# Performance work log

Measured on AMD Instinct MI355X. Metric: run time of the kernel, lower is better.

## Reference

```python
import jax, jax.numpy as jnp
import numpy as np

N = 50000
E = 800000
IN_DIM = 128
HID = 64


def _glorot(key, shape):
    fan_in, fan_out = shape[0], shape[-1]
    lim = jnp.sqrt(6.0 / (fan_in + fan_out))
    return jax.random.uniform(key, shape, jnp.float32, -lim, lim)


def setup_inputs() -> dict:
    key = jax.random.key(0)
    ks = jax.random.split(key, 12)
    x = jax.random.normal(ks[0], (N, IN_DIM), jnp.float32)
    edge_index = jax.random.randint(ks[1], (2, E), 0, N, jnp.int64)
    return {
        "x": x,
        "edge_index": edge_index,
        # GATConv 1: in=128 -> 64 per head, 4 heads (concat -> 256)
        "W1": _glorot(ks[2], (IN_DIM, 4 * HID)),
        "a_src1": _glorot(ks[3], (4, HID)),
        "a_dst1": _glorot(ks[4], (4, HID)),
        "b1": jnp.zeros((4 * HID,), jnp.float32),
        # GATConv 2: in=256 -> 64, 1 head
        "W2": _glorot(ks[5], (4 * HID, HID)),
        "a_src2": _glorot(ks[6], (1, HID)),
        "a_dst2": _glorot(ks[7], (1, HID)),
        "b2": jnp.zeros((HID,), jnp.float32),
        # classifier 64 -> 32 -> 2
        "W3": _glorot(ks[8], (HID, 32)),
        "b3": jnp.zeros((32,), jnp.float32),
        "W4": _glorot(ks[9], (32, 2)),
        "b4": jnp.zeros((2,), jnp.float32),
    }


def _gat_layer(x, edge_index, W, a_src, a_dst, b, heads, out_ch):
    """PyG-style GATConv (add_self_loops=True, negative_slope=0.2, concat)."""
    n = x.shape[0]
    loop = jnp.arange(n, dtype=edge_index.dtype)
    src = jnp.concatenate([edge_index[0], loop])  # [E+N]
    dst = jnp.concatenate([edge_index[1], loop])
    h = (x @ W).reshape(n, heads, out_ch)  # [N,H,C]
    as_ = jnp.sum(h * a_src[None], axis=-1)  # [N,H]
    ad_ = jnp.sum(h * a_dst[None], axis=-1)  # [N,H]
    e = jax.nn.leaky_relu(as_[src] + ad_[dst], negative_slope=0.2)  # [E+N,H]
    # segment softmax over destination nodes
    m = jax.ops.segment_max(e, dst, num_segments=n)  # [N,H]
    ex = jnp.exp(e - m[dst])
    s = jax.ops.segment_sum(ex, dst, num_segments=n)
    alpha = ex / (s[dst] + 1e-16)  # [E+N,H]
    msg = h[src] * alpha[:, :, None]  # [E+N,H,C]
    out = jax.ops.segment_sum(msg, dst, num_segments=n)  # [N,H,C]
    return out.reshape(n, heads * out_ch) + b


def reference(x, edge_index, W1, a_src1, a_dst1, b1, W2, a_src2, a_dst2, b2, W3, b3, W4, b4):
    h = jax.nn.elu(_gat_layer(x, edge_index, W1, a_src1, a_dst1, b1, heads=4, out_ch=HID))
    h = jax.nn.elu(_gat_layer(h, edge_index, W2, a_src2, a_dst2, b2, heads=1, out_ch=HID))
    h = jax.nn.relu(h @ W3 + b3)
    return h @ W4 + b4  # [N, 2] logits
```

## Files before the change

### kernel.cpp

```cpp
#include <hip/hip_runtime.h>
#include <math.h>

#define NNODES 50000
#define NEDGES 800000
#define CAP 128

typedef __attribute__((ext_vector_type(8))) short bfrag8;
typedef __attribute__((ext_vector_type(4))) float f32x4;

__device__ __forceinline__ unsigned short f2bf(float f) {
    unsigned b = __float_as_uint(f);
    b += 0x7fffu + ((b >> 16) & 1u);
    return (unsigned short)(b >> 16);
}
__device__ __forceinline__ float bf_lo(unsigned u) { return __uint_as_float(u << 16); }
__device__ __forceinline__ float bf_hi(unsigned u) { return __uint_as_float(u & 0xffff0000u); }

__device__ __forceinline__ void pack_one(const float* W, unsigned short* Wp, int K, int NC,
                                         int idx) {
    int k = idx / NC, n = idx % NC;
    int kf = k >> 5, q = (k >> 3) & 3, j = k & 7;
    Wp[((((size_t)n * (K >> 5) + kf) * 4 + q) << 3) + j] = f2bf(W[idx]);
}

__global__ void prep_kernel(const float* __restrict__ x, unsigned short* __restrict__ xb,
                            const float* __restrict__ W1, unsigned short* __restrict__ W1p,
                            const float* __restrict__ W2, unsigned short* __restrict__ W2p,
                            int* __restrict__ cnt, int ncvt4, int n) {
    int idx = blockIdx.x * blockDim.x + threadIdx.x;
    if (idx < ncvt4) {
        float4 v = *(const float4*)&x[idx * 4];
        ushort4 s;
        s.x = f2bf(v.x); s.y = f2bf(v.y); s.z = f2bf(v.z); s.w = f2bf(v.w);
        *(ushort4*)&xb[idx * 4] = s;
    }
    if (idx < 128 * 256) pack_one(W1, W1p, 128, 256, idx);
    if (idx < 256 * 64) pack_one(W2, W2p, 256, 64, idx);
    if (idx < n) cnt[idx] = 0;
}

template <int K, int H>
__device__ __forceinline__ void gemm_dev(const unsigned short* __restrict__ Ab,
                                         const unsigned short* __restrict__ Bp,
                                         const float* __restrict__ a_src,
                                         const float* __restrict__ a_dst,
                                         unsigned short* __restrict__ Cb,
                                         float* __restrict__ as_, float* __restrict__ ad_,
                                         int M, int bid) {
    constexpr int KF = K / 32;
    constexpr int NC = H * 64;
    int wave = threadIdx.x >> 6, lane = threadIdx.x & 63;
    int m0 = (bid * 4 + wave) * 16;
    if (m0 >= M) return;
    int quad = lane >> 4, l16 = lane & 15;
    int row = m0 + l16;

    bfrag8 a[KF];
    const unsigned short* arow = Ab + (size_t)row * K + quad * 8;
#pragma unroll
    for (int f = 0; f < KF; f++) a[f] = *(const bfrag8*)(arow + f * 32);

    float ps[4] = {0.f, 0.f, 0.f, 0.f};
    float pd[4] = {0.f, 0.f, 0.f, 0.f};
#pragma unroll
    for (int nt = 0; nt < NC / 16; nt++) {
        f32x4 acc = {0.f, 0.f, 0.f, 0.f};
        const unsigned short* bp = Bp + (((size_t)(nt * 16 + l16) * KF) * 4 + quad) * 8;
#pragma unroll
        for (int f = 0; f < KF; f++) {
            bfrag8 bfr = *(const bfrag8*)(bp + (size_t)f * 32);
            acc = __builtin_amdgcn_mfma_f32_16x16x32_bf16(a[f], bfr, acc, 0, 0, 0);
        }
        int col = nt * 16 + l16;
        float avs = a_src[col], avd = a_dst[col];
#pragma unroll
        for (int r = 0; r < 4; r++) {
            ps[r] = fmaf(acc[r], avs, ps[r]);
            pd[r] = fmaf(acc[r], avd, pd[r]);
            unsigned pk = (unsigned)f2bf(acc[r]) |
                          ((unsigned)f2bf(__shfl_down(acc[r], 1)) << 16);
            if (!(l16 & 1))
                *(unsigned*)&Cb[(size_t)(m0 + quad * 4 + r) * NC + nt * 16 + l16] = pk;
        }
        if ((nt & 3) == 3) {
            int head = nt >> 2;
#pragma unroll
            for (int off = 1; off < 16; off <<= 1) {
#pragma unroll
                for (int r = 0; r < 4; r++) {
                    ps[r] += __shfl_xor(ps[r], off);
                    pd[r] += __shfl_xor(pd[r], off);
                }
            }
            if (l16 == 0) {
#pragma unroll
                for (int r = 0; r < 4; r++) {
                    as_[(size_t)(m0 + quad * 4 + r) * H + head] = ps[r];
                    ad_[(size_t)(m0 + quad * 4 + r) * H + head] = pd[r];
                }
            }
#pragma unroll
            for (int r = 0; r < 4; r++) { ps[r] = 0.f; pd[r] = 0.f; }
        }
    }
}

__global__ __launch_bounds__(256) void gemm1_scatter(
    const unsigned short* __restrict__ xb, const unsigned short* __restrict__ W1p,
    const float* __restrict__ a_src1, const float* __restrict__ a_dst1,
    unsigned short* __restrict__ h1b, float* __restrict__ as1, float* __restrict__ ad1,
    const int* __restrict__ ei, int* __restrict__ cnt, int* __restrict__ bucket,
    int M, int GB, int nE, int nT) {
    if ((int)blockIdx.x < GB) {
        gemm_dev<128, 4>(xb, W1p, a_src1, a_dst1, h1b, as1, ad1, M, blockIdx.x);
    } else {
        int idx = (blockIdx.x - GB) * 256 + threadIdx.x;
        if (idx >= nT) return;
        int src, dst;
        if (idx < nE) { src = ei[idx]; dst = ei[nE + idx]; } else { src = dst = idx - nE; }
        int slot = atomicAdd(&cnt[dst], 1);
        if (slot < CAP) bucket[(size_t)dst * CAP + slot] = src;
    }
}

__global__ __launch_bounds__(256) void gemm2_kernel(
    const unsigned short* __restrict__ Ab, const unsigned short* __restrict__ Bp,
    const float* __restrict__ a_src, const float* __restrict__ a_dst,
    unsigned short* __restrict__ Cb, float* __restrict__ as_, float* __restrict__ ad_,
    int M) {
    gemm_dev<256, 1>(Ab, Bp, a_src, a_dst, Cb, as_, ad_, M, blockIdx.x);
}

__global__ void node_agg4(const int* __restrict__ cnt, const int* __restrict__ bucket,
                          const float* __restrict__ as_, const float* __restrict__ ad_,
                          const unsigned short* __restrict__ hb, const float* __restrict__ b,
                          unsigned short* __restrict__ outb, int n) {
    __shared__ float alf[4][64][4];
    __shared__ int srs[4][64];
    int w = threadIdx.x >> 6;
    int node = blockIdx.x * 4 + w;
    int lane = threadIdx.x & 63;
    if (node >= n) return;
    int cntAll = cnt[node];
    if (cntAll > CAP) cntAll = CAP;
    const int* bkt = bucket + (size_t)node * CAP;
    int cnt0 = cntAll < 64 ? cntAll : 64;
    bool v0 = lane < cnt0;
    int half = lane >> 5;
    int hl = lane & 31;
    int head = hl >> 3;
    int ch0 = hl * 8;

    float4 adv = *(const float4*)&ad_[node * 4];
    float adn[4] = {adv.x, adv.y, adv.z, adv.w};

    int src0 = bkt[v0 ? lane : 0];
    float4 asv = *(const float4*)&as_[src0 * 4];
    float ev[4];
    {
        float e0 = asv.x + adn[0], e1 = asv.y + adn[1];
        float e2 = asv.z + adn[2], e3 = asv.w + adn[3];
        ev[0] = e0 > 0.f ? e0 : 0.2f * e0;
        ev[1] = e1 > 0.f ? e1 : 0.2f * e1;
        ev[2] = e2 > 0.f ? e2 : 0.2f * e2;
        ev[3] = e3 > 0.f ? e3 : 0.2f * e3;
    }
    float mx[4];
#pragma unroll
    for (int h = 0; h < 4; h++) mx[h] = v0 ? ev[h] : -1e30f;

    bool hv2 = false;
    int src2 = 0;
    float e2v[4] = {0.f, 0.f, 0.f, 0.f};
    if (cntAll > 64) {
        int i2 = 64 + lane;
        hv2 = i2 < cntAll;
        src2 = bkt[hv2 ? i2 : 0];
        float4 a2 = *(const float4*)&as_[src2 * 4];
        float t0 = a2.x + adn[0], t1 = a2.y + adn[1];
        float t2 = a2.z + adn[2], t3 = a2.w + adn[3];
        e2v[0] = t0 > 0.f ? t0 : 0.2f * t0;
        e2v[1] = t1 > 0.f ? t1 : 0.2f * t1;
        e2v[2] = t2 > 0.f ? t2 : 0.2f * t2;
        e2v[3] = t3 > 0.f ? t3 : 0.2f * t3;
        if (hv2) {
#pragma unroll
            for (int h = 0; h < 4; h++) mx[h] = fmaxf(mx[h], e2v[h]);
        }
    }
#pragma unroll
    for (int off = 32; off > 0; off >>= 1) {
#pragma unroll
        for (int h = 0; h < 4; h++) mx[h] = fmaxf(mx[h], __shfl_xor(mx[h], off));
    }
    float x0[4], sl[4], x2[4];
#pragma unroll
    for (int h = 0; h < 4; h++) {
        x0[h] = v0 ? __expf(ev[h] - mx[h]) : 0.f;
        sl[h] = x0[h];
        x2[h] = 0.f;
    }
    if (cntAll > 64 && hv2) {
#pragma unroll
        for (int h = 0; h < 4; h++) {
            x2[h] = __expf(e2v[h] - mx[h]);
            sl[h] += x2[h];
        }
    }
#pragma unroll
    for (int off = 32; off > 0; off >>= 1) {
#pragma unroll
        for (int h = 0; h < 4; h++) sl[h] += __shfl_xor(sl[h], off);
    }
    float inv_s[4];
#pragma unroll
    for (int h = 0; h < 4; h++) inv_s[h] = 1.f / (sl[h] + 1e-16f);

    srs[w][lane] = src0;
    {
        float4 mal;
        mal.x = x0[0] * inv_s[0];
        mal.y = x0[1] * inv_s[1];
        mal.z = x0[2] * inv_s[2];
        mal.w = x0[3] * inv_s[3];
        *(float4*)&alf[w][lane][0] = mal;
    }

    float acc[8];
#pragma unroll
    for (int k = 0; k < 8; k++) acc[k] = 0.f;

    int iters = (cnt0 + 1) >> 1;
    int iters4 = (iters + 3) & ~3;

#define LD4(vk, ak, t)                                              \
    {                                                               \
        int e_ = 2 * (t) + half;                                    \
        int s_ = srs[w][e_];                                        \
        ak = alf[w][e_][head];                                      \
        vk = *(const uint4*)&hb[(size_t)s_ * 256 + ch0];            \
    }
#define FMA8(ak, vk)                                                \
    {                                                               \
        acc[0] = fmaf(ak, bf_lo(vk.x), acc[0]);                     \
        acc[1] = fmaf(ak, bf_hi(vk.x), acc[1]);                     \
        acc[2] = fmaf(ak, bf_lo(vk.y), acc[2]);                     \
        acc[3] = fmaf(ak, bf_hi(vk.y), acc[3]);                     \
        acc[4] = fmaf(ak, bf_lo(vk.z), acc[4]);                     \
        acc[5] = fmaf(ak, bf_hi(vk.z), acc[5]);                     \
        acc[6] = fmaf(ak, bf_lo(vk.w), acc[6]);                     \
        acc[7] = fmaf(ak, bf_hi(vk.w), acc[7]);                     \
    }

    uint4 q0, q1, q2, q3;
    float a0, a1, a2, a3;
    LD4(q0, a0, 0) LD4(q1, a1, 1) LD4(q2, a2, 2) LD4(q3, a3, 3)
    int c = 0;
    for (; c < iters4 - 4; c += 4) {
        FMA8(a0, q0) LD4(q0, a0, c + 4)
        FMA8(a1, q1) LD4(q1, a1, c + 5)
        FMA8(a2, q2) LD4(q2, a2, c + 6)
        FMA8(a3, q3) LD4(q3, a3, c + 7)
    }
    FMA8(a0, q0) FMA8(a1, q1) FMA8(a2, q2) FMA8(a3, q3)

    if (cntAll > 64) {
        srs[w][lane] = src2;
        float4 m2v;
        m2v.x = x2[0] * inv_s[0];
        m2v.y = x2[1] * inv_s[1];
        m2v.z = x2[2] * inv_s[2];
        m2v.w = x2[3] * inv_s[3];
        *(float4*)&alf[w][lane][0] = m2v;
        int c2 = cntAll - 64;
        for (int j = 0; j < c2; j += 2) {
            int e_ = j + half;
            int s_ = srs[w][e_];
            float al = alf[w][e_][head];
            uint4 v = *(const uint4*)&hb[(size_t)s_ * 256 + ch0];
            FMA8(al, v)
        }
    }
#pragma unroll
    for (int k = 0; k < 8; k++) acc[k] += __shfl_down(acc[k], 32);
    if (half == 0) {
        float4 b0 = *(const float4*)&b[ch0];
        float4 b1 = *(const float4*)&b[ch0 + 4];
        float o[8] = {acc[0] + b0.x, acc[1] + b0.y, acc[2] + b0.z, acc[3] + b0.w,
                      acc[4] + b1.x, acc[5] + b1.y, acc[6] + b1.z, acc[7] + b1.w};
#pragma unroll
        for (int k = 0; k < 8; k++) o[k] = o[k] > 0.f ? o[k] : __expf(o[k]) - 1.f;
        uint4 p;
        p.x = f2bf(o[0]) | ((unsigned)f2bf(o[1]) << 16);
        p.y = f2bf(o[2]) | ((unsigned)f2bf(o[3]) << 16);
        p.z = f2bf(o[4]) | ((unsigned)f2bf(o[5]) << 16);
        p.w = f2bf(o[6]) | ((unsigned)f2bf(o[7]) << 16);
        *(uint4*)&outb[(size_t)node * 256 + ch0] = p;
    }
#undef LD4
#undef FMA8
}

__global__ void node_agg1_cls(const int* __restrict__ cnt, const int* __restrict__ bucket,
                              const float* __restrict__ as_, const float* __restrict__ ad_,
                              const unsigned short* __restrict__ hb,
                              const float* __restrict__ b2v,
                              const float* __restrict__ W3, const float* __restrict__ b3,
                              const float* __restrict__ W4, const float* __restrict__ b4,
                              float* __restrict__ out, int n) {
    __shared__ float alf[4][64];
    __shared__ int srs[4][64];
    __shared__ float w3s[2048];
    __shared__ float w4s[64], b3s[32], b4s[2];
    __shared__ float zrow[4][64];
    __shared__ float hrow[4][32];
    int tid = threadIdx.x;
    int w = tid >> 6;
    int lane = tid & 63;
#pragma unroll
    for (int i = 0; i < 8; i++) w3s[i * 256 + tid] = W3[i * 256 + tid];
    if (tid < 64) w4s[tid] = W4[tid];
    if (tid < 32) b3s[tid] = b3[tid];
    if (tid < 2) b4s[tid] = b4[tid];
    __syncthreads();

    int node = blockIdx.x * 4 + w;
    if (node >= n) return;
    int cntAll = cnt[node];
    if (cntAll > CAP) cntAll = CAP;
    const int* bkt = bucket + (size_t)node * CAP;
    int cnt0 = cntAll < 64 ? cntAll : 64;
    bool v0 = lane < cnt0;
    int q = lane >> 4;
    int ql = lane & 15;
    int ch0 = ql * 4;

    float adn = ad_[node];
    int src0 = bkt[v0 ? lane : 0];
    float ev = as_[src0] + adn;
    ev = ev > 0.f ? ev : 0.2f * ev;
    float mx = v0 ? ev : -1e30f;

    bool hv2 = false;
    int src2 = 0;
    float e2v = 0.f;
    if (cntAll > 64) {
        int i2 = 64 + lane;
        hv2 = i2 < cntAll;
        src2 = bkt[hv2 ? i2 : 0];
        float t = as_[src2] + adn;
        e2v = t > 0.f ? t : 0.2f * t;
        if (hv2) mx = fmaxf(mx, e2v);
    }
#pragma unroll
    for (int off = 32; off > 0; off >>= 1) mx = fmaxf(mx, __shfl_xor(mx, off));
    float x0 = v0 ? __expf(ev - mx) : 0.f;
    float sl = x0;
    float x2 = 0.f;
    if (cntAll > 64 && hv2) {
        x2 = __expf(e2v - mx);
        sl += x2;
    }
#pragma unroll
    for (int off = 32; off > 0; off >>= 1) sl += __shfl_xor(sl, off);
    float inv_s = 1.f / (sl + 1e-16f);

    srs[w][lane] = src0;
    alf[w][lane] = x0 * inv_s;

    float acc[4] = {0.f, 0.f, 0.f, 0.f};
    int iters = (cnt0 + 3) >> 2;
    int iters4 = (iters + 3) & ~3;

#define LD2(vk, ak, t)                                              \
    {                                                               \
        int e_ = 4 * (t) + q;                                       \
        int s_ = srs[w][e_];                                        \
        ak = alf[w][e_];                                            \
        vk = *(const uint2*)&hb[(size_t)s_ * 64 + ch0];             \
    }
#define FMA4(ak, vk)                                                \
    {                                                               \
        acc[0] = fmaf(ak, bf_lo(vk.x), acc[0]);                     \
        acc[1] = fmaf(ak, bf_hi(vk.x), acc[1]);                     \
        acc[2] = fmaf(ak, bf_lo(vk.y), acc[2]);                     \
        acc[3] = fmaf(ak, bf_hi(vk.y), acc[3]);                     \
    }

    uint2 q0, q1, q2, q3;
    float a0, a1, a2, a3;
    LD2(q0, a0, 0) LD2(q1, a1, 1) LD2(q2, a2, 2) LD2(q3, a3, 3)
    int c = 0;
    for (; c < iters4 - 4; c += 4) {
        FMA4(a0, q0) LD2(q0, a0, c + 4)
        FMA4(a1, q1) LD2(q1, a1, c + 5)
        FMA4(a2, q2) LD2(q2, a2, c + 6)
        FMA4(a3, q3) LD2(q3, a3, c + 7)
    }
    FMA4(a0, q0) FMA4(a1, q1) FMA4(a2, q2) FMA4(a3, q3)

    if (cntAll > 64) {
        srs[w][lane] = src2;
        alf[w][lane] = x2 * inv_s;
        int c2 = cntAll - 64;
        for (int j = 0; j < c2; j += 4) {
            int e_ = j + q;
            int s_ = srs[w][e_];
            float al = alf[w][e_];
            uint2 v = *(const uint2*)&hb[(size_t)s_ * 64 + ch0];
            FMA4(al, v)
        }
    }
#pragma unroll
    for (int k = 0; k < 4; k++) {
        acc[k] += __shfl_down(acc[k], 32);
        acc[k] += __shfl_down(acc[k], 16);
    }
    if (q == 0) {
        float4 bv = *(const float4*)&b2v[ch0];
        float o0 = acc[0] + bv.x, o1 = acc[1] + bv.y, o2 = acc[2] + bv.z, o3 = acc[3] + bv.w;
        zrow[w][ch0 + 0] = o0 > 0.f ? o0 : __expf(o0) - 1.f;
        zrow[w][ch0 + 1] = o1 > 0.f ? o1 : __expf(o1) - 1.f;
        zrow[w][ch0 + 2] = o2 > 0.f ? o2 : __expf(o2) - 1.f;
        zrow[w][ch0 + 3] = o3 > 0.f ? o3 : __expf(o3) - 1.f;
    }
    {
        int p = lane & 1, j = lane >> 1;
        float partial = 0.f;
#pragma unroll
        for (int i = 0; i < 32; i++) {
            int k = p * 32 + i;
            partial = fmaf(zrow[w][k], w3s[k * 32 + j], partial);
        }
        partial += __shfl_down(partial, 1);
        if (p == 0) {
            float hv = partial + b3s[j];
            hrow[w][j] = hv > 0.f ? hv : 0.f;
        }
    }
    if (lane < 2) {
        float o = b4s[lane];
#pragma unroll
        for (int j = 0; j < 32; j++) o = fmaf(hrow[w][j], w4s[j * 2 + lane], o);
        out[(size_t)node * 2 + lane] = o;
    }
#undef LD2
#undef FMA4
}

extern "C" void kernel_launch(void* const* d_in, const int* in_sizes, int n_in,
                              void* d_out, int out_size, void* d_ws, size_t ws_size,
                              hipStream_t stream) {
    const float* x      = (const float*)d_in[0];
    const int*   ei     = (const int*)d_in[1];
    const float* W1     = (const float*)d_in[2];
    const float* a_src1 = (const float*)d_in[3];
    const float* a_dst1 = (const float*)d_in[4];
    const float* b1     = (const float*)d_in[5];
    const float* W2     = (const float*)d_in[6];
    const float* a_src2 = (const float*)d_in[7];
    const float* a_dst2 = (const float*)d_in[8];
    const float* b2     = (const float*)d_in[9];
    const float* W3     = (const float*)d_in[10];
    const float* b3     = (const float*)d_in[11];
    const float* W4     = (const float*)d_in[12];
    const float* b4     = (const float*)d_in[13];
    float* out = (float*)d_out;

    const int N = NNODES, E = NEDGES, ET = E + N;

    float* ws = (float*)d_ws;
    size_t o = 0;
    float* as1  = ws + o; o += (size_t)N * 4;
    float* ad1  = ws + o; o += (size_t)N * 4;
    unsigned short* h1b   = (unsigned short*)(ws + o); o += (size_t)N * 128;
    unsigned short* h2b   = (unsigned short*)(ws + o); o += (size_t)N * 32;
    unsigned short* out1b = (unsigned short*)(ws + o); o += (size_t)N * 128;
    unsigned short* xb    = (unsigned short*)(ws + o); o += (size_t)N * 64;
    unsigned short* W1p   = (unsigned short*)(ws + o); o += 16384;
    unsigned short* W2p   = (unsigned short*)(ws + o); o += 8192;
    int* cnt    = (int*)(ws + o); o += N;
    int* bucket = (int*)(ws + o); o += (size_t)N * CAP;

    dim3 blk(256);

    const int NCVT4 = N * 128 / 4;
    prep_kernel<<<(NCVT4 + 255) / 256, blk, 0, stream>>>(x, xb, W1, W1p, W2, W2p, cnt,
                                                         NCVT4, N);

    const int GB = (N + 63) / 64;
    const int SB = (ET + 255) / 256;
    gemm1_scatter<<<GB + SB, blk, 0, stream>>>(xb, W1p, a_src1, a_dst1, h1b, as1, ad1,
                                               ei, cnt, bucket, N, GB, E, ET);

    node_agg4<<<(N + 3) / 4, blk, 0, stream>>>(cnt, bucket, as1, ad1, h1b, b1, out1b, N);

    gemm2_kernel<<<GB, blk, 0, stream>>>(out1b, W2p, a_src2, a_dst2, h2b, as1, ad1, N);

    node_agg1_cls<<<(N + 3) / 4, blk, 0, stream>>>(cnt, bucket, as1, ad1, h2b, b2, W3, b3,
                                                   W4, b4, out, N);
}
```

Before: 316.1 us.

## Two-level binned edge bucketing and deferred softmax normalization without max

Edge bucketing now runs in two stages. Edges are first appended to coarse 64-node bins with global atomics, then a new per-bin kernel distributes them into per-node buckets using shared-memory atomics. This is meant to reduce global atomic contention on per-node counters, at the cost of an extra kernel launch and an extra pass over the edge list. The aggregation kernels also drop the max-subtraction step of the segment softmax and apply the 1/sum normalization after accumulation. That removes a shuffle reduction and the per-edge scaling, but risks exp overflow for large attention logits.

```diff
diff --git a/kernel.cpp b/kernel.cpp
--- a/kernel.cpp
+++ b/kernel.cpp
@@ -4,6 +4,8 @@
 #define NNODES 50000
 #define NEDGES 800000
 #define CAP 128
+#define NBIN 782
+#define BINCAP 2048
 
 typedef __attribute__((ext_vector_type(8))) short bfrag8;
 typedef __attribute__((ext_vector_type(4))) float f32x4;
@@ -26,7 +28,7 @@
 __global__ void prep_kernel(const float* __restrict__ x, unsigned short* __restrict__ xb,
                             const float* __restrict__ W1, unsigned short* __restrict__ W1p,
                             const float* __restrict__ W2, unsigned short* __restrict__ W2p,
-                            int* __restrict__ cnt, int ncvt4, int n) {
+                            int* __restrict__ bincnt, int ncvt4) {
     int idx = blockIdx.x * blockDim.x + threadIdx.x;
     if (idx < ncvt4) {
         float4 v = *(const float4*)&x[idx * 4];
@@ -36,7 +38,7 @@
     }
     if (idx < 128 * 256) pack_one(W1, W1p, 128, 256, idx);
     if (idx < 256 * 64) pack_one(W2, W2p, 256, 64, idx);
-    if (idx < n) cnt[idx] = 0;
+    if (idx < NBIN) bincnt[idx] = 0;
 }
 
 template <int K, int H>
@@ -105,11 +107,11 @@
     }
 }
 
-__global__ __launch_bounds__(256) void gemm1_scatter(
+__global__ __launch_bounds__(256) void gemm1_binA(
     const unsigned short* __restrict__ xb, const unsigned short* __restrict__ W1p,
     const float* __restrict__ a_src1, const float* __restrict__ a_dst1,
     unsigned short* __restrict__ h1b, float* __restrict__ as1, float* __restrict__ ad1,
-    const int* __restrict__ ei, int* __restrict__ cnt, int* __restrict__ bucket,
+    const int* __restrict__ ei, int* __restrict__ bincnt, int* __restrict__ bindata,
     int M, int GB, int nE, int nT) {
     if ((int)blockIdx.x < GB) {
         gemm_dev<128, 4>(xb, W1p, a_src1, a_dst1, h1b, as1, ad1, M, blockIdx.x);
@@ -118,9 +120,33 @@
         if (idx >= nT) return;
         int src, dst;
         if (idx < nE) { src = ei[idx]; dst = ei[nE + idx]; } else { src = dst = idx - nE; }
-        int slot = atomicAdd(&cnt[dst], 1);
-        if (slot < CAP) bucket[(size_t)dst * CAP + slot] = src;
-    }
+        int b = dst >> 6;
+        int slot = atomicAdd(&bincnt[b], 1);
+        if (slot < BINCAP) bindata[(size_t)b * BINCAP + slot] = src | ((dst & 63) << 16);
+    }
+}
+
+__global__ __launch_bounds__(256) void bin_to_bucket(const int* __restrict__ bincnt,
+                                                     const int* __restrict__ bindata,
+                                                     int* __restrict__ cnt,
+                                                     int* __restrict__ bucket, int n) {
+    __shared__ int lc[64];
+    int b = blockIdx.x, t = threadIdx.x;
+    if (t < 64) lc[t] = 0;
+    __syncthreads();
+    int nb = bincnt[b];
+    if (nb > BINCAP) nb = BINCAP;
+    int base = b * 64;
+    const int* bd = bindata + (size_t)b * BINCAP;
+    for (int i = t; i < nb; i += 256) {
+        int pk = bd[i];
+        int src = pk & 0xFFFF;
+        int dstl = pk >> 16;
+        int slot = atomicAdd(&lc[dstl], 1);
+        if (slot < CAP) bucket[(size_t)(base + dstl) * CAP + slot] = src;
+    }
+    __syncthreads();
+    if (t < 64 && base + t < n) cnt[base + t] = lc[t];
 }
 
 __global__ __launch_bounds__(256) void gemm2_kernel(
@@ -156,22 +182,22 @@
 
     int src0 = bkt[v0 ? lane : 0];
     float4 asv = *(const float4*)&as_[src0 * 4];
-    float ev[4];
+    float x0[4];
     {
         float e0 = asv.x + adn[0], e1 = asv.y + adn[1];
         float e2 = asv.z + adn[2], e3 = asv.w + adn[3];
-        ev[0] = e0 > 0.f ? e0 : 0.2f * e0;
-        ev[1] = e1 > 0.f ? e1 : 0.2f * e1;
-        ev[2] = e2 > 0.f ? e2 : 0.2f * e2;
-        ev[3] = e3 > 0.f ? e3 : 0.2f * e3;
-    }
-    float mx[4];
-#pragma unroll
-    for (int h = 0; h < 4; h++) mx[h] = v0 ? ev[h] : -1e30f;
-
+        e0 = e0 > 0.f ? e0 : 0.2f * e0;
+        e1 = e1 > 0.f ? e1 : 0.2f * e1;
+        e2 = e2 > 0.f ? e2 : 0.2f * e2;
+        e3 = e3 > 0.f ? e3 : 0.2f * e3;
+        x0[0] = v0 ? __expf(e0) : 0.f;
+        x0[1] = v0 ? __expf(e1) : 0.f;
+        x0[2] = v0 ? __expf(e2) : 0.f;
+        x0[3] = v0 ? __expf(e3) : 0.f;
+    }
     bool hv2 = false;
     int src2 = 0;
-    float e2v[4] = {0.f, 0.f, 0.f, 0.f};
+    float x2[4] = {0.f, 0.f, 0.f, 0.f};
     if (cntAll > 64) {
         int i2 = 64 + lane;
         hv2 = i2 < cntAll;
@@ -179,52 +205,17 @@
         float4 a2 = *(const float4*)&as_[src2 * 4];
         float t0 = a2.x + adn[0], t1 = a2.y + adn[1];
         float t2 = a2.z + adn[2], t3 = a2.w + adn[3];
-        e2v[0] = t0 > 0.f ? t0 : 0.2f * t0;
-        e2v[1] = t1 > 0.f ? t1 : 0.2f * t1;
-        e2v[2] = t2 > 0.f ? t2 : 0.2f * t2;
-        e2v[3] = t3 > 0.f ? t3 : 0.2f * t3;
-        if (hv2) {
-#pragma unroll
-            for (int h = 0; h < 4; h++) mx[h] = fmaxf(mx[h], e2v[h]);
-        }
-    }
-#pragma unroll
-    for (int off = 32; off > 0; off >>= 1) {
-#pragma unroll
-        for (int h = 0; h < 4; h++) mx[h] = fmaxf(mx[h], __shfl_xor(mx[h], off));
-    }
-    float x0[4], sl[4], x2[4];
-#pragma unroll
-    for (int h = 0; h < 4; h++) {
-        x0[h] = v0 ? __expf(ev[h] - mx[h]) : 0.f;
-        sl[h] = x0[h];
-        x2[h] = 0.f;
-    }
-    if (cntAll > 64 && hv2) {
-#pragma unroll
-        for (int h = 0; h < 4; h++) {
-            x2[h] = __expf(e2v[h] - mx[h]);
-            sl[h] += x2[h];
-        }
-    }
-#pragma unroll
-    for (int off = 32; off > 0; off >>= 1) {
-#pragma unroll
-        for (int h = 0; h < 4; h++) sl[h] += __shfl_xor(sl[h], off);
-    }
-    float inv_s[4];
-#pragma unroll
-    for (int h = 0; h < 4; h++) inv_s[h] = 1.f / (sl[h] + 1e-16f);
-
+        t0 = t0 > 0.f ? t0 : 0.2f * t0;
+        t1 = t1 > 0.f ? t1 : 0.2f * t1;
+        t2 = t2 > 0.f ? t2 : 0.2f * t2;
+        t3 = t3 > 0.f ? t3 : 0.2f * t3;
+        x2[0] = hv2 ? __expf(t0) : 0.f;
+        x2[1] = hv2 ? __expf(t1) : 0.f;
+        x2[2] = hv2 ? __expf(t2) : 0.f;
+        x2[3] = hv2 ? __expf(t3) : 0.f;
+    }
     srs[w][lane] = src0;
-    {
-        float4 mal;
-        mal.x = x0[0] * inv_s[0];
-        mal.y = x0[1] * inv_s[1];
-        mal.z = x0[2] * inv_s[2];
-        mal.w = x0[3] * inv_s[3];
-        *(float4*)&alf[w][lane][0] = mal;
-    }
+    *(float4*)&alf[w][lane][0] = make_float4(x0[0], x0[1], x0[2], x0[3]);
 
     float acc[8];
 #pragma unroll
@@ -266,12 +257,7 @@
 
     if (cntAll > 64) {
         srs[w][lane] = src2;
-        float4 m2v;
-        m2v.x = x2[0] * inv_s[0];
-        m2v.y = x2[1] * inv_s[1];
-        m2v.z = x2[2] * inv_s[2];
-        m2v.w = x2[3] * inv_s[3];
-        *(float4*)&alf[w][lane][0] = m2v;
+        *(float4*)&alf[w][lane][0] = make_float4(x2[0], x2[1], x2[2], x2[3]);
         int c2 = cntAll - 64;
         for (int j = 0; j < c2; j += 2) {
             int e_ = j + half;
@@ -281,13 +267,25 @@
             FMA8(al, v)
         }
     }
+    float sl[4];
+#pragma unroll
+    for (int h = 0; h < 4; h++) sl[h] = x0[h] + x2[h];
+#pragma unroll
+    for (int off = 32; off > 0; off >>= 1) {
+#pragma unroll
+        for (int h = 0; h < 4; h++) sl[h] += __shfl_xor(sl[h], off);
+    }
+    float inv_h = 1.f / (sl[head] + 1e-16f);
+
 #pragma unroll
     for (int k = 0; k < 8; k++) acc[k] += __shfl_down(acc[k], 32);
     if (half == 0) {
         float4 b0 = *(const float4*)&b[ch0];
         float4 b1 = *(const float4*)&b[ch0 + 4];
-        float o[8] = {acc[0] + b0.x, acc[1] + b0.y, acc[2] + b0.z, acc[3] + b0.w,
-                      acc[4] + b1.x, acc[5] + b1.y, acc[6] + b1.z, acc[7] + b1.w};
+        float o[8] = {fmaf(acc[0], inv_h, b0.x), fmaf(acc[1], inv_h, b0.y),
+                      fmaf(acc[2], inv_h, b0.z), fmaf(acc[3], inv_h, b0.w),
+                      fmaf(acc[4], inv_h, b1.x), fmaf(acc[5], inv_h, b1.y),
+                      fmaf(acc[6], inv_h, b1.z), fmaf(acc[7], inv_h, b1.w)};
 #pragma unroll
         for (int k = 0; k < 8; k++) o[k] = o[k] > 0.f ? o[k] : __expf(o[k]) - 1.f;
         uint4 p;
@@ -339,34 +337,21 @@
     int src0 = bkt[v0 ? lane : 0];
     float ev = as_[src0] + adn;
     ev = ev > 0.f ? ev : 0.2f * ev;
-    float mx = v0 ? ev : -1e30f;
+    float x0 = v0 ? __expf(ev) : 0.f;
 
     bool hv2 = false;
     int src2 = 0;
-    float e2v = 0.f;
+    float x2 = 0.f;
     if (cntAll > 64) {
         int i2 = 64 + lane;
         hv2 = i2 < cntAll;
         src2 = bkt[hv2 ? i2 : 0];
         float t = as_[src2] + adn;
-        e2v = t > 0.f ? t : 0.2f * t;
-        if (hv2) mx = fmaxf(mx, e2v);
-    }
-#pragma unroll
-    for (int off = 32; off > 0; off >>= 1) mx = fmaxf(mx, __shfl_xor(mx, off));
-    float x0 = v0 ? __expf(ev - mx) : 0.f;
-    float sl = x0;
-    float x2 = 0.f;
-    if (cntAll > 64 && hv2) {
-        x2 = __expf(e2v - mx);
-        sl += x2;
-    }
-#pragma unroll
-    for (int off = 32; off > 0; off >>= 1) sl += __shfl_xor(sl, off);
-    float inv_s = 1.f / (sl + 1e-16f);
-
+        t = t > 0.f ? t : 0.2f * t;
+        x2 = hv2 ? __expf(t) : 0.f;
+    }
     srs[w][lane] = src0;
-    alf[w][lane] = x0 * inv_s;
+    alf[w][lane] = x0;
 
     float acc[4] = {0.f, 0.f, 0.f, 0.f};
     int iters = (cnt0 + 3) >> 2;
@@ -401,7 +386,7 @@
 
     if (cntAll > 64) {
         srs[w][lane] = src2;
-        alf[w][lane] = x2 * inv_s;
+        alf[w][lane] = x2;
         int c2 = cntAll - 64;
         for (int j = 0; j < c2; j += 4) {
             int e_ = j + q;
@@ -411,6 +396,11 @@
             FMA4(al, v)
         }
     }
+    float sl = x0 + x2;
+#pragma unroll
+    for (int off = 32; off > 0; off >>= 1) sl += __shfl_xor(sl, off);
+    float inv_s = 1.f / (sl + 1e-16f);
+
 #pragma unroll
     for (int k = 0; k < 4; k++) {
         acc[k] += __shfl_down(acc[k], 32);
@@ -418,7 +408,8 @@
     }
     if (q == 0) {
         float4 bv = *(const float4*)&b2v[ch0];
-        float o0 = acc[0] + bv.x, o1 = acc[1] + bv.y, o2 = acc[2] + bv.z, o3 = acc[3] + bv.w;
+        float o0 = fmaf(acc[0], inv_s, bv.x), o1 = fmaf(acc[1], inv_s, bv.y);
+        float o2 = fmaf(acc[2], inv_s, bv.z), o3 = fmaf(acc[3], inv_s, bv.w);
         zrow[w][ch0 + 0] = o0 > 0.f ? o0 : __expf(o0) - 1.f;
         zrow[w][ch0 + 1] = o1 > 0.f ? o1 : __expf(o1) - 1.f;
         zrow[w][ch0 + 2] = o2 > 0.f ? o2 : __expf(o2) - 1.f;
@@ -479,19 +470,23 @@
     unsigned short* xb    = (unsigned short*)(ws + o); o += (size_t)N * 64;
     unsigned short* W1p   = (unsigned short*)(ws + o); o += 16384;
     unsigned short* W2p   = (unsigned short*)(ws + o); o += 8192;
-    int* cnt    = (int*)(ws + o); o += N;
-    int* bucket = (int*)(ws + o); o += (size_t)N * CAP;
+    int* cnt     = (int*)(ws + o); o += N;
+    int* bucket  = (int*)(ws + o); o += (size_t)N * CAP;
+    int* bincnt  = (int*)(ws + o); o += 1024;
+    int* bindata = (int*)(ws + o); o += (size_t)NBIN * BINCAP;
 
     dim3 blk(256);
 
     const int NCVT4 = N * 128 / 4;
-    prep_kernel<<<(NCVT4 + 255) / 256, blk, 0, stream>>>(x, xb, W1, W1p, W2, W2p, cnt,
-                                                         NCVT4, N);
+    prep_kernel<<<(NCVT4 + 255) / 256, blk, 0, stream>>>(x, xb, W1, W1p, W2, W2p, bincnt,
+                                                         NCVT4);
 
     const int GB = (N + 63) / 64;
     const int SB = (ET + 255) / 256;
-    gemm1_scatter<<<GB + SB, blk, 0, stream>>>(xb, W1p, a_src1, a_dst1, h1b, as1, ad1,
-                                               ei, cnt, bucket, N, GB, E, ET);
+    gemm1_binA<<<GB + SB, blk, 0, stream>>>(xb, W1p, a_src1, a_dst1, h1b, as1, ad1,
+                                            ei, bincnt, bindata, N, GB, E, ET);
+
+    bin_to_bucket<<<NBIN, blk, 0, stream>>>(bincnt, bindata, cnt, bucket, N);
 
     node_agg4<<<(N + 3) / 4, blk, 0, stream>>>(cnt, bucket, as1, ad1, h1b, b1, out1b, N);
 
```

After: 470.1 us. 1.49x slower.
